# Optimization experiments

Measured on AMD Instinct MI355X. Metric: run time of the kernel, lower is better.

## Reference

```python
import jax, jax.numpy as jnp
import numpy as np

NEG_SLOPE = 0.2  # PyG GATConv default leaky_relu slope


def gat_conv(h_in, src, dst, W, a_src, a_dst, b, N):
    # h_in: [N, Fin]; src/dst: [E] (self-loops already appended)
    h = h_in @ W                      # [N, Fout]
    alpha_src = h @ a_src             # [N]
    alpha_dst = h @ a_dst             # [N]
    e = jax.nn.leaky_relu(alpha_src[src] + alpha_dst[dst], NEG_SLOPE)  # [E]
    # segment softmax over incoming edges of each destination node
    m = jax.ops.segment_max(e, dst, num_segments=N)
    m = jnp.where(jnp.isfinite(m), m, 0.0)
    p = jnp.exp(e - m[dst])
    denom = jax.ops.segment_sum(p, dst, num_segments=N)
    alpha = p / jnp.maximum(denom[dst], 1e-16)
    out = jax.ops.segment_sum(alpha[:, None] * h[src], dst, num_segments=N)
    return out + b


def setup_inputs() -> dict:
    key = jax.random.key(0)
    ks = jax.random.split(key, 16)
    N, E, V, D, H, C, G = 100000, 1600000, 128, 50, 16, 10, 512
    x = jax.random.normal(ks[0], (N, V), dtype=jnp.float32)
    edge_index = jax.random.randint(ks[1], (2, E), 0, N, dtype=jnp.int32)
    batch = jnp.sort(jax.random.randint(ks[2], (N,), 0, G, dtype=jnp.int32))
    s = lambda fan: 1.0 / np.sqrt(fan)
    return {
        "x": x, "edge_index": edge_index, "batch": batch,
        "embedding": jax.random.normal(ks[3], (V, D), dtype=jnp.float32),
        "W1": jax.random.normal(ks[4], (D, H), dtype=jnp.float32) * s(D),
        "a_src1": jax.random.normal(ks[5], (H,), dtype=jnp.float32) * s(H),
        "a_dst1": jax.random.normal(ks[6], (H,), dtype=jnp.float32) * s(H),
        "b1": jnp.zeros((H,), dtype=jnp.float32),
        "W2": jax.random.normal(ks[7], (H, H), dtype=jnp.float32) * s(H),
        "a_src2": jax.random.normal(ks[8], (H,), dtype=jnp.float32) * s(H),
        "a_dst2": jax.random.normal(ks[9], (H,), dtype=jnp.float32) * s(H),
        "b2": jnp.zeros((H,), dtype=jnp.float32),
        "W3": jax.random.normal(ks[10], (H, C), dtype=jnp.float32) * s(H),
        "a_src3": jax.random.normal(ks[11], (C,), dtype=jnp.float32) * s(C),
        "a_dst3": jax.random.normal(ks[12], (C,), dtype=jnp.float32) * s(C),
        "b3": jnp.zeros((C,), dtype=jnp.float32),
    }


def reference(x, edge_index, batch, embedding, W1, a_src1, a_dst1, b1,
              W2, a_src2, a_dst2, b2, W3, a_src3, a_dst3, b3):
    N = x.shape[0]
    G = 512  # num graphs
    # embedding lookup via argmax over one-hot-ish features
    idx = jnp.argmax(x, axis=1)
    h = embedding[idx]                               # [N, 50]
    # add self-loops once (PyG GATConv default)
    loops = jnp.arange(N, dtype=edge_index.dtype)
    src = jnp.concatenate([edge_index[0], loops])
    dst = jnp.concatenate([edge_index[1], loops])
    h = jax.nn.relu(gat_conv(h, src, dst, W1, a_src1, a_dst1, b1, N))
    # dropout: eval mode -> identity
    h = jax.nn.relu(gat_conv(h, src, dst, W2, a_src2, a_dst2, b2, N))
    h = gat_conv(h, src, dst, W3, a_src3, a_dst3, b3, N)  # [N, C]
    # global mean pool over graphs
    sums = jax.ops.segment_sum(h, batch, num_segments=G)
    cnts = jax.ops.segment_sum(jnp.ones((N,), h.dtype), batch, num_segments=G)
    pooled = sums / jnp.maximum(cnts, 1.0)[:, None]
    return jax.nn.softmax(pooled, axis=1)
```

## Files before the change

kernel.cpp:

```cpp
#include <hip/hip_runtime.h>
#include <math.h>

#define NEG_SLOPE 0.2f
#define NBUK_MAX 2048

__global__ void k_argmax(const float* __restrict__ x, int* __restrict__ idx, int N, int V) {
    int node = (blockIdx.x * blockDim.x + threadIdx.x) >> 5;
    int lane = threadIdx.x & 31;
    if (node >= N) return;
    const float4* row = (const float4*)(x + (long long)node * V);
    float bv = -INFINITY;
    int bi = 0x7fffffff;
    int nq = V >> 2;
    for (int q = lane; q < nq; q += 32) {
        float4 v = row[q];
        int base = q << 2;
        if (v.x > bv || (v.x == bv && base     < bi)) { bv = v.x; bi = base;     }
        if (v.y > bv || (v.y == bv && base + 1 < bi)) { bv = v.y; bi = base + 1; }
        if (v.z > bv || (v.z == bv && base + 2 < bi)) { bv = v.z; bi = base + 2; }
        if (v.w > bv || (v.w == bv && base + 3 < bi)) { bv = v.w; bi = base + 3; }
    }
    for (int off = 16; off > 0; off >>= 1) {
        float ov = __shfl_down(bv, off, 32);
        int   oi = __shfl_down(bi, off, 32);
        if (ov > bv || (ov == bv && oi < bi)) { bv = ov; bi = oi; }
    }
    if (lane == 0) idx[node] = bi;
}

template <int FIN, int FOUT, bool GATHER>
__global__ void k_transform(const float* __restrict__ h_in, const int* __restrict__ idx,
                            const float* __restrict__ W,
                            const float* __restrict__ a_src, const float* __restrict__ a_dst,
                            _Float16* __restrict__ h_t, float* __restrict__ asrc,
                            float* __restrict__ adst, int N) {
    __shared__ float sW[FIN * FOUT];
    __shared__ float sa[FOUT], sd[FOUT];
    for (int i = threadIdx.x; i < FIN * FOUT; i += blockDim.x) sW[i] = W[i];
    if (threadIdx.x < FOUT) { sa[threadIdx.x] = a_src[threadIdx.x]; sd[threadIdx.x] = a_dst[threadIdx.x]; }
    __syncthreads();
    int n = blockIdx.x * blockDim.x + threadIdx.x;
    if (n >= N) return;
    float acc[FOUT];
#pragma unroll
    for (int f = 0; f < FOUT; f++) acc[f] = 0.f;
    const float* hr = GATHER ? (h_in + (long long)idx[n] * FIN)
                             : (h_in + (long long)n * FIN);
    for (int k = 0; k < FIN; k++) {
        float v = hr[k];
#pragma unroll
        for (int f = 0; f < FOUT; f++) acc[f] += v * sW[k * FOUT + f];
    }
    float s1 = 0.f, s2 = 0.f;
    _Float16 hh[16];
#pragma unroll
    for (int f = 0; f < 16; f++) hh[f] = (_Float16)0.f;
#pragma unroll
    for (int f = 0; f < FOUT; f++) {
        hh[f] = (_Float16)acc[f];
        s1 += acc[f] * sa[f];
        s2 += acc[f] * sd[f];
    }
    uint4* dst = (uint4*)(h_t + (long long)n * 16);
    dst[0] = ((uint4*)hh)[0];
    dst[1] = ((uint4*)hh)[1];
    asrc[n] = s1;
    adst[n] = s2;
}

template <int B2>
__global__ void __launch_bounds__(1024)
k_histB(const int* __restrict__ edst, int E, int* __restrict__ histT, int NBUK) {
    __shared__ int sh[NBUK_MAX];
    int t = threadIdx.x, b = blockIdx.x;
    for (int k = t; k < NBUK; k += 1024) sh[k] = 0;
    __syncthreads();
    long long ebeg = (long long)b * E / B2, eend = (long long)(b + 1) * E / B2;
    for (long long i = ebeg + t; i < eend; i += 1024)
        atomicAdd(&sh[edst[i] >> 6], 1);
    __syncthreads();
    for (int k = t; k < NBUK; k += 1024) histT[(long long)k * B2 + b] = sh[k];
}

__global__ void k_scan1(const int* __restrict__ vals, int* __restrict__ excl,
                        int* __restrict__ bsums, int M) {
    __shared__ int s[256];
    int i = blockIdx.x * 256 + threadIdx.x;
    int v = (i < M) ? vals[i] : 0;
    s[threadIdx.x] = v;
    __syncthreads();
    for (int off = 1; off < 256; off <<= 1) {
        int a = (threadIdx.x >= (unsigned)off) ? s[threadIdx.x - off] : 0;
        __syncthreads();
        s[threadIdx.x] += a;
        __syncthreads();
    }
    if (i < M) excl[i] = s[threadIdx.x] - v;
    if (threadIdx.x == 255) bsums[blockIdx.x] = s[255];
}

__global__ void k_scan2(int* __restrict__ bsums, int nb) {
    __shared__ int s[2048];
    int i = threadIdx.x;
    int v0 = (i < nb) ? bsums[i] : 0;
    int v1 = (i + 1024 < nb) ? bsums[i + 1024] : 0;
    s[i] = v0;
    s[i + 1024] = v1;
    __syncthreads();
    for (int off = 1; off < 2048; off <<= 1) {
        int a0 = (i >= off) ? s[i - off] : 0;
        int a1 = (i + 1024 >= off) ? s[i + 1024 - off] : 0;
        __syncthreads();
        s[i] += a0;
        s[i + 1024] += a1;
        __syncthreads();
    }
    if (i < nb) bsums[i] = s[i] - v0;
    if (i + 1024 < nb) bsums[i + 1024] = s[i + 1024] - v1;
}

template <int B2>
__global__ void __launch_bounds__(1024)
k_scatB(const int* __restrict__ esrc, const int* __restrict__ edst, int E,
        const int* __restrict__ sexcl, const int* __restrict__ bsums,
        int* __restrict__ tmp, int NBUK) {
    __shared__ int cur[NBUK_MAX];
    int t = threadIdx.x, b = blockIdx.x;
    for (int k = t; k < NBUK; k += 1024)
        cur[k] = sexcl[(long long)k * B2 + b] + bsums[k];
    __syncthreads();
    long long ebeg = (long long)b * E / B2, eend = (long long)(b + 1) * E / B2;
    for (long long i = ebeg + t; i < eend; i += 1024) {
        int d = edst[i];
        int pos = atomicAdd(&cur[d >> 6], 1);
        tmp[pos] = ((d & 63) << 18) | esrc[i];
    }
}

template <int B2>
__global__ void __launch_bounds__(256)
k_binB(const int* __restrict__ sexcl, const int* __restrict__ bsums,
       const int* __restrict__ tmp,
       int* __restrict__ rowptr, int* __restrict__ csr_src, int N, int NBUK, int E) {
    __shared__ int cnt[64];
    __shared__ int cur[64];
    int t = threadIdx.x, b = blockIdx.x;
    int t0 = sexcl[(long long)b * B2] + bsums[b];
    int t1 = (b + 1 < NBUK) ? (sexcl[(long long)(b + 1) * B2] + bsums[b + 1]) : E;
    if (t < 64) cnt[t] = 0;
    __syncthreads();
    for (int i = t0 + t; i < t1; i += 256) atomicAdd(&cnt[tmp[i] >> 18], 1);
    __syncthreads();
    if (t < 64) {
        int v = cnt[t];
        int incl = v;
        for (int off = 1; off < 64; off <<= 1) {
            int u = __shfl_up(incl, off, 64);
            if (t >= off) incl += u;
        }
        int base = t0 + incl - v;
        int d = (b << 6) + t;
        if (d < N) rowptr[d] = base;
        cur[t] = base;
        if (d == N - 1) rowptr[N] = E;
    }
    __syncthreads();
    for (int i = t0 + t; i < t1; i += 256) {
        int p = tmp[i];
        int pos = atomicAdd(&cur[p >> 18], 1);
        csr_src[pos] = p & 0x3FFFF;
    }
}

template <int FOUT, bool BIAS, bool RELU>
__global__ void k_gat_dst(const int* __restrict__ rowptr, const int* __restrict__ csr_src,
                          const float* __restrict__ asrc, const float* __restrict__ adst,
                          const _Float16* __restrict__ h_t, const float* __restrict__ b,
                          float* __restrict__ out, int N) {
    int grp  = (blockIdx.x * blockDim.x + threadIdx.x) >> 4;
    int lane = threadIdx.x & 15;
    if (grp >= N) return;
    int d = grp;
    int r0 = rowptr[d], r1 = rowptr[d + 1];
    float ad = adst[d];
    constexpr bool FULL = (FOUT == 16);
    const bool active = FULL || lane < FOUT;

    float e0 = asrc[d] + ad;
    e0 = (e0 >= 0.f) ? e0 : NEG_SLOPE * e0;
    float p0 = __expf(e0);
    float acc  = p0 * (float)h_t[(long long)d * 16 + lane];
    float psum = (lane == 0) ? p0 : 0.f;

    int j = r0;
    if (j < r1) {
        int myj = j + lane;
        bool valid = myj < r1;
        int s = valid ? csr_src[myj] : d;
        float a = asrc[s];
        while (true) {
            int jn = j + 16;
            int s2 = d; float a2 = 0.f; bool validn = false;
            if (jn < r1) {
                int myjn = jn + lane;
                validn = myjn < r1;
                s2 = validn ? csr_src[myjn] : d;
                a2 = asrc[s2];
            }
            float e = a + ad;
            e = (e >= 0.f) ? e : NEG_SLOPE * e;
            float p = valid ? __expf(e) : 0.f;
            psum += p;
#pragma unroll
            for (int k = 0; k < 16; k++) {
                float pk = __shfl(p, k, 16);
                int   sk = __shfl(s, k, 16);
                acc += pk * (float)h_t[(long long)sk * 16 + lane];
            }
            if (jn >= r1) break;
            j = jn; s = s2; a = a2; valid = validn;
        }
    }
    for (int off = 8; off > 0; off >>= 1) psum += __shfl_xor(psum, off, 16);

    if (active) {
        float v = acc / fmaxf(psum, 1e-16f);
        if (BIAS) v += b[lane];
        if (RELU) v = fmaxf(v, 0.f);
        out[(long long)d * FOUT + lane] = v;
    }
}

__global__ void k_pool(const float* __restrict__ h3, const int* __restrict__ batch,
                       const float* __restrict__ b3, float* __restrict__ out, int N, int C) {
    int g = blockIdx.x;
    int lo = 0, hi = N;
    while (lo < hi) { int mid = (lo + hi) >> 1; if (batch[mid] < g) lo = mid + 1; else hi = mid; }
    int start = lo;
    hi = N;
    while (lo < hi) { int mid = (lo + hi) >> 1; if (batch[mid] < g + 1) lo = mid + 1; else hi = mid; }
    int end = lo;

    float sum[16];
    for (int f = 0; f < C; f++) sum[f] = 0.f;
    for (int n = start + threadIdx.x; n < end; n += blockDim.x) {
        const float* r = h3 + (long long)n * C;
        for (int f = 0; f < C; f++) sum[f] += r[f];
    }
    __shared__ float red[256 * 16];
    for (int f = 0; f < C; f++) red[threadIdx.x * 16 + f] = sum[f];
    __syncthreads();
    for (int str = blockDim.x / 2; str > 0; str >>= 1) {
        if ((int)threadIdx.x < str)
            for (int f = 0; f < C; f++) red[threadIdx.x * 16 + f] += red[(threadIdx.x + str) * 16 + f];
        __syncthreads();
    }
    if (threadIdx.x == 0) {
        float cnt = fmaxf((float)(end - start), 1.f);
        float vals[16];
        float mx = -INFINITY;
        for (int f = 0; f < C; f++) { vals[f] = red[f] / cnt + b3[f]; mx = fmaxf(mx, vals[f]); }
        float se = 0.f;
        for (int f = 0; f < C; f++) { vals[f] = __expf(vals[f] - mx); se += vals[f]; }
        for (int f = 0; f < C; f++) out[(long long)g * C + f] = vals[f] / se;
    }
}

extern "C" void kernel_launch(void* const* d_in, const int* in_sizes, int n_in,
                              void* d_out, int out_size, void* d_ws, size_t ws_size,
                              hipStream_t stream) {
    const float* x    = (const float*)d_in[0];
    const int*   eidx = (const int*)d_in[1];
    const int*   batch= (const int*)d_in[2];
    const float* emb  = (const float*)d_in[3];
    const float* W1   = (const float*)d_in[4];
    const float* as1  = (const float*)d_in[5];
    const float* ad1  = (const float*)d_in[6];
    const float* b1   = (const float*)d_in[7];
    const float* W2   = (const float*)d_in[8];
    const float* as2  = (const float*)d_in[9];
    const float* ad2  = (const float*)d_in[10];
    const float* b2   = (const float*)d_in[11];
    const float* W3   = (const float*)d_in[12];
    const float* as3  = (const float*)d_in[13];
    const float* ad3  = (const float*)d_in[14];
    const float* b3   = (const float*)d_in[15];

    const int H = in_sizes[5];
    const int C = in_sizes[13];
    const int D = in_sizes[4] / H;
    const int V = in_sizes[3] / D;
    const int N = in_sizes[0] / V;
    const int E = in_sizes[1] / 2;
    const int G = out_size / C;
    const int* esrc = eidx;
    const int* edst = eidx + E;
    const int NBUK = (N + 63) >> 6;
    constexpr int B2 = 256;
    const int M = NBUK * B2;

    char* w = (char*)d_ws;
    auto carve = [&](size_t bytes) {
        char* p = w;
        w += (bytes + 255) & ~(size_t)255;
        return p;
    };
    float*     asrc    = (float*)carve((size_t)N * 4);
    float*     adst    = (float*)carve((size_t)N * 4);
    int*       idx     = (int*)carve((size_t)N * 4);
    int*       rowptr  = (int*)carve((size_t)(N + 1) * 4);
    int*       csr_src = (int*)carve((size_t)E * 4);
    int*       histT   = (int*)carve((size_t)M * 4);
    int*       sexcl   = (int*)carve((size_t)M * 4);
    int*       bsums   = (int*)carve(2048 * 4);
    _Float16*  hT      = (_Float16*)carve((size_t)N * 16 * 2);
    char*  zone = w;
    float* X0 = (float*)zone;
    float* X1 = (float*)(zone + (((size_t)N * H * 4 + 255) & ~(size_t)255));
    int*   tmp = (int*)zone;
    (void)ws_size; (void)n_in;

    const int BT = 256;
    dim3 blk(BT);
    int gN   = (N + BT - 1) / BT;
    int gArg = (N * 32 + BT - 1) / BT;
    int gGat = (N * 16 + BT - 1) / BT;
    int nb2  = (M + 255) / 256;

    k_histB<B2><<<B2, dim3(1024), 0, stream>>>(edst, E, histT, NBUK);
    k_scan1<<<nb2, blk, 0, stream>>>(histT, sexcl, bsums, M);
    k_scan2<<<1, 1024, 0, stream>>>(bsums, nb2);
    k_scatB<B2><<<B2, dim3(1024), 0, stream>>>(esrc, edst, E, sexcl, bsums, tmp, NBUK);
    k_binB<B2><<<NBUK, blk, 0, stream>>>(sexcl, bsums, tmp, rowptr, csr_src, N, NBUK, E);

    k_argmax<<<gArg, blk, 0, stream>>>(x, idx, N, V);

    k_transform<50, 16, true><<<gN, blk, 0, stream>>>(emb, idx, W1, as1, ad1, hT, asrc, adst, N);
    k_gat_dst<16, true, true><<<gGat, blk, 0, stream>>>(rowptr, csr_src, asrc, adst, hT, b1, X0, N);

    k_transform<16, 16, false><<<gN, blk, 0, stream>>>(X0, nullptr, W2, as2, ad2, hT, asrc, adst, N);
    k_gat_dst<16, true, true><<<gGat, blk, 0, stream>>>(rowptr, csr_src, asrc, adst, hT, b2, X1, N);

    k_transform<16, 10, false><<<gN, blk, 0, stream>>>(X1, nullptr, W3, as3, ad3, hT, asrc, adst, N);
    k_gat_dst<10, false, false><<<gGat, blk, 0, stream>>>(rowptr, csr_src, asrc, adst, hT, nullptr, X0, N);

    k_pool<<<G, blk, 0, stream>>>(X0, batch, b3, (float*)d_out, N, C);
}
```

Measured before the change: 274.1 us.

## Fuse next-layer linear transform and attention logits into GAT aggregation epilogue

Each GAT aggregation kernel for layers 1 and 2 now applies bias and ReLU, then multiplies by the next layer's weight matrix using lane shuffles. It also reduces the next layer's source and destination attention coefficients and writes the fp16 features directly. This removes two standalone transform kernels and their fp32 intermediate round-trips through memory. Ping-pong buffers are added for features and coefficients, at the cost of extra shuffles and shared-memory weight loads in every aggregation block.

```diff
diff --git a/kernel.cpp b/kernel.cpp
--- a/kernel.cpp
+++ b/kernel.cpp
@@ -28,7 +28,7 @@
     if (lane == 0) idx[node] = bi;
 }
 
-template <int FIN, int FOUT, bool GATHER>
+template <int FIN, int FOUT>
 __global__ void k_transform(const float* __restrict__ h_in, const int* __restrict__ idx,
                             const float* __restrict__ W,
                             const float* __restrict__ a_src, const float* __restrict__ a_dst,
@@ -44,8 +44,7 @@
     float acc[FOUT];
 #pragma unroll
     for (int f = 0; f < FOUT; f++) acc[f] = 0.f;
-    const float* hr = GATHER ? (h_in + (long long)idx[n] * FIN)
-                             : (h_in + (long long)n * FIN);
+    const float* hr = h_in + (long long)idx[n] * FIN;
     for (int k = 0; k < FIN; k++) {
         float v = hr[k];
 #pragma unroll
@@ -172,19 +171,16 @@
     }
 }
 
-template <int FOUT, bool BIAS, bool RELU>
-__global__ void k_gat_dst(const int* __restrict__ rowptr, const int* __restrict__ csr_src,
-                          const float* __restrict__ asrc, const float* __restrict__ adst,
-                          const _Float16* __restrict__ h_t, const float* __restrict__ b,
-                          float* __restrict__ out, int N) {
-    int grp  = (blockIdx.x * blockDim.x + threadIdx.x) >> 4;
-    int lane = threadIdx.x & 15;
-    if (grp >= N) return;
+template <typename EPI>
+__device__ __forceinline__ void gat_core(const int* __restrict__ rowptr,
+                                         const int* __restrict__ csr_src,
+                                         const float* __restrict__ asrc,
+                                         const float* __restrict__ adst,
+                                         const _Float16* __restrict__ h_t,
+                                         int N, int grp, int lane, EPI epilogue) {
     int d = grp;
     int r0 = rowptr[d], r1 = rowptr[d + 1];
     float ad = adst[d];
-    constexpr bool FULL = (FOUT == 16);
-    const bool active = FULL || lane < FOUT;
 
     float e0 = asrc[d] + ad;
     e0 = (e0 >= 0.f) ? e0 : NEG_SLOPE * e0;
@@ -222,13 +218,59 @@
         }
     }
     for (int off = 8; off > 0; off >>= 1) psum += __shfl_xor(psum, off, 16);
-
-    if (active) {
-        float v = acc / fmaxf(psum, 1e-16f);
-        if (BIAS) v += b[lane];
-        if (RELU) v = fmaxf(v, 0.f);
-        out[(long long)d * FOUT + lane] = v;
-    }
+    epilogue(d, acc / fmaxf(psum, 1e-16f));
+}
+
+template <int FN>
+__global__ void k_gat_ft(const int* __restrict__ rowptr, const int* __restrict__ csr_src,
+                         const float* __restrict__ asrc, const float* __restrict__ adst,
+                         const _Float16* __restrict__ h_t, const float* __restrict__ bias,
+                         const float* __restrict__ Wn, const float* __restrict__ an_src,
+                         const float* __restrict__ an_dst,
+                         _Float16* __restrict__ h_next, float* __restrict__ asrc_n,
+                         float* __restrict__ adst_n, int N) {
+    __shared__ float sW[16 * FN];
+    __shared__ float sa[FN], sd[FN], sb[16];
+    for (int i = threadIdx.x; i < 16 * FN; i += blockDim.x) sW[i] = Wn[i];
+    if (threadIdx.x < FN) { sa[threadIdx.x] = an_src[threadIdx.x]; sd[threadIdx.x] = an_dst[threadIdx.x]; }
+    if (threadIdx.x < 16) sb[threadIdx.x] = bias[threadIdx.x];
+    __syncthreads();
+
+    int grp  = (blockIdx.x * blockDim.x + threadIdx.x) >> 4;
+    int lane = threadIdx.x & 15;
+    if (grp >= N) return;
+
+    gat_core(rowptr, csr_src, asrc, adst, h_t, N, grp, lane,
+        [&](int d, float v) {
+            v = fmaxf(v + sb[lane], 0.f);
+            float acc2 = 0.f;
+#pragma unroll
+            for (int k = 0; k < 16; k++) {
+                float vk = __shfl(v, k, 16);
+                if (lane < FN) acc2 += vk * sW[k * FN + lane];
+            }
+            float c1 = (lane < FN) ? acc2 * sa[lane] : 0.f;
+            float c2 = (lane < FN) ? acc2 * sd[lane] : 0.f;
+            for (int off = 8; off > 0; off >>= 1) {
+                c1 += __shfl_xor(c1, off, 16);
+                c2 += __shfl_xor(c2, off, 16);
+            }
+            h_next[(long long)d * 16 + lane] = (_Float16)((lane < FN) ? acc2 : 0.f);
+            if (lane == 0) { asrc_n[d] = c1; adst_n[d] = c2; }
+        });
+}
+
+template <int FOUT>
+__global__ void k_gat_last(const int* __restrict__ rowptr, const int* __restrict__ csr_src,
+                           const float* __restrict__ asrc, const float* __restrict__ adst,
+                           const _Float16* __restrict__ h_t, float* __restrict__ out, int N) {
+    int grp  = (blockIdx.x * blockDim.x + threadIdx.x) >> 4;
+    int lane = threadIdx.x & 15;
+    if (grp >= N) return;
+    gat_core(rowptr, csr_src, asrc, adst, h_t, N, grp, lane,
+        [&](int d, float v) {
+            if (lane < FOUT) out[(long long)d * FOUT + lane] = v;
+        });
 }
 
 __global__ void k_pool(const float* __restrict__ h3, const int* __restrict__ batch,
@@ -305,18 +347,21 @@
         w += (bytes + 255) & ~(size_t)255;
         return p;
     };
-    float*     asrc    = (float*)carve((size_t)N * 4);
-    float*     adst    = (float*)carve((size_t)N * 4);
+    float*     as_a    = (float*)carve((size_t)N * 4);
+    float*     ad_a    = (float*)carve((size_t)N * 4);
+    float*     as_b    = (float*)carve((size_t)N * 4);
+    float*     ad_b    = (float*)carve((size_t)N * 4);
     int*       idx     = (int*)carve((size_t)N * 4);
     int*       rowptr  = (int*)carve((size_t)(N + 1) * 4);
     int*       csr_src = (int*)carve((size_t)E * 4);
     int*       histT   = (int*)carve((size_t)M * 4);
     int*       sexcl   = (int*)carve((size_t)M * 4);
     int*       bsums   = (int*)carve(2048 * 4);
-    _Float16*  hT      = (_Float16*)carve((size_t)N * 16 * 2);
-    char*  zone = w;
-    float* X0 = (float*)zone;
-    float* X1 = (float*)(zone + (((size_t)N * H * 4 + 255) & ~(size_t)255));
+    _Float16*  hTa     = (_Float16*)carve((size_t)N * 16 * 2);
+    _Float16*  hTb     = (_Float16*)carve((size_t)N * 16 * 2);
+    size_t zone_bytes = ((size_t)E * 4 > (size_t)N * C * 4) ? (size_t)E * 4 : (size_t)N * C * 4;
+    char*  zone = carve(zone_bytes);
+    float* X0  = (float*)zone;
     int*   tmp = (int*)zone;
     (void)ws_size; (void)n_in;
 
@@ -334,15 +379,15 @@
     k_binB<B2><<<NBUK, blk, 0, stream>>>(sexcl, bsums, tmp, rowptr, csr_src, N, NBUK, E);
 
     k_argmax<<<gArg, blk, 0, stream>>>(x, idx, N, V);
-
-    k_transform<50, 16, true><<<gN, blk, 0, stream>>>(emb, idx, W1, as1, ad1, hT, asrc, adst, N);
-    k_gat_dst<16, true, true><<<gGat, blk, 0, stream>>>(rowptr, csr_src, asrc, adst, hT, b1, X0, N);
-
-    k_transform<16, 16, false><<<gN, blk, 0, stream>>>(X0, nullptr, W2, as2, ad2, hT, asrc, adst, N);
-    k_gat_dst<16, true, true><<<gGat, blk, 0, stream>>>(rowptr, csr_src, asrc, adst, hT, b2, X1, N);
-
-    k_transform<16, 10, false><<<gN, blk, 0, stream>>>(X1, nullptr, W3, as3, ad3, hT, asrc, adst, N);
-    k_gat_dst<10, false, false><<<gGat, blk, 0, stream>>>(rowptr, csr_src, asrc, adst, hT, nullptr, X0, N);
+    k_transform<50, 16><<<gN, blk, 0, stream>>>(emb, idx, W1, as1, ad1, hTa, as_a, ad_a, N);
+
+    k_gat_ft<16><<<gGat, blk, 0, stream>>>(rowptr, csr_src, as_a, ad_a, hTa, b1,
+                                           W2, as2, ad2, hTb, as_b, ad_b, N);
+
+    k_gat_ft<10><<<gGat, blk, 0, stream>>>(rowptr, csr_src, as_b, ad_b, hTb, b2,
+                                           W3, as3, ad3, hTa, as_a, ad_a, N);
+
+    k_gat_last<10><<<gGat, blk, 0, stream>>>(rowptr, csr_src, as_a, ad_a, hTa, X0, N);
 
     k_pool<<<G, blk, 0, stream>>>(X0, batch, b3, (float*)d_out, N, C);
 }
```

Result: no change. 275.7 us (+0.6%).
